# Kernel optimization log

Hardware: AMD Instinct MI355X
Metric: run time of the kernel (lower is better)

Reference implementation:

```python
import jax, jax.numpy as jnp
import numpy as np

N = 100000   # nodes
E = 1600000  # edges (avg degree 16)
D = 128      # embed_dim
H1, C1 = 8, 16   # gat1: heads=8, out=embed_dim//8=16, concat -> 128
C2 = 32          # gat2: heads=1, out=32
NEG_SLOPE = 0.2  # PyG GATConv default leaky relu slope


def _gat_layer(x, src, dst, W, a_src, a_dst, b, heads, ch, concat):
    """PyG-style GATConv (eval mode, add_self_loops already applied via src/dst)."""
    n = x.shape[0]
    h = (x @ W).reshape(n, heads, ch)                      # [N,H,C]
    alpha_s = jnp.einsum('nhc,hc->nh', h, a_src)           # [N,H]
    alpha_d = jnp.einsum('nhc,hc->nh', h, a_dst)           # [N,H]
    e = jax.nn.leaky_relu(alpha_s[src] + alpha_d[dst], NEG_SLOPE)  # [Etot,H]
    # segment softmax over incoming edges of each dst node
    m = jax.ops.segment_max(e, dst, num_segments=n)        # [N,H]
    ex = jnp.exp(e - m[dst])
    s = jax.ops.segment_sum(ex, dst, num_segments=n)       # [N,H]
    alpha = ex / (s[dst] + 1e-16)                          # [Etot,H]
    out = jax.ops.segment_sum(alpha[:, :, None] * h[src], dst, num_segments=n)  # [N,H,C]
    out = out.reshape(n, heads * ch) if concat else out.mean(axis=1)
    return out + b


def setup_inputs():
    key = jax.random.key(0)
    ks = jax.random.split(key, 12)
    x = jax.random.normal(ks[0], (N, D), dtype=jnp.float32)
    edge_index = jax.random.randint(ks[1], (2, E), 0, N, dtype=jnp.int64)
    sc = 0.1
    W1 = jax.random.normal(ks[2], (D, H1 * C1), jnp.float32) * sc
    a1_src = jax.random.normal(ks[3], (H1, C1), jnp.float32) * sc
    a1_dst = jax.random.normal(ks[4], (H1, C1), jnp.float32) * sc
    b1 = jnp.zeros((H1 * C1,), jnp.float32)
    W2 = jax.random.normal(ks[5], (H1 * C1, C2), jnp.float32) * sc
    a2_src = jax.random.normal(ks[6], (1, C2), jnp.float32) * sc
    a2_dst = jax.random.normal(ks[7], (1, C2), jnp.float32) * sc
    b2 = jnp.zeros((C2,), jnp.float32)
    Wh = jax.random.normal(ks[8], (C2, 1), jnp.float32) * sc
    bh = jnp.zeros((1,), jnp.float32)
    return {"x": x, "edge_index": edge_index,
            "W1": W1, "a1_src": a1_src, "a1_dst": a1_dst, "b1": b1,
            "W2": W2, "a2_src": a2_src, "a2_dst": a2_dst, "b2": b2,
            "Wh": Wh, "bh": bh}


def reference(x, edge_index, W1, a1_src, a1_dst, b1, W2, a2_src, a2_dst, b2, Wh, bh):
    n = x.shape[0]
    loops = jnp.arange(n, dtype=edge_index.dtype)
    src = jnp.concatenate([edge_index[0], loops])  # add_self_loops=True (PyG default)
    dst = jnp.concatenate([edge_index[1], loops])
    h = jax.nn.elu(_gat_layer(x, src, dst, W1, a1_src, a1_dst, b1, H1, C1, True))
    h = jax.nn.elu(_gat_layer(h, src, dst, W2, a2_src, a2_dst, b2, 1, C2, False))
    return h @ Wh + bh  # [N,1] ordinal head
```

## Files before the change

### kernel.cpp

```cpp
#include <hip/hip_runtime.h>
#include <hip/hip_bf16.h>
#include <stdint.h>
#include <stddef.h>

#define NEG_SLOPE 0.2f
#define XS 136

#define NBK   196
#define BWSH  9
#define BCAP  12288
#define NPREP 64

typedef __bf16 bf16x8 __attribute__((ext_vector_type(8)));
typedef float  f32x4  __attribute__((ext_vector_type(4)));

__device__ __forceinline__ float bf2f(__hip_bfloat16 b){ return __bfloat162float(b); }
__device__ __forceinline__ float lo_bf(unsigned u){ return __uint_as_float(u << 16); }
__device__ __forceinline__ float hi_bf(unsigned u){ return __uint_as_float(u & 0xffff0000u); }
__device__ __forceinline__ float lrelu(float u){ return fmaxf(u, NEG_SLOPE * u); }
__device__ __forceinline__ unsigned short f2bf(float f){
    unsigned u = __float_as_uint(f);
    return (unsigned short)((u + 0x7fffu + ((u >> 16) & 1u)) >> 16);
}
__device__ __forceinline__ float bfs2f(unsigned short s){ return __uint_as_float((unsigned)s << 16); }
__device__ __forceinline__ float ldraw(const void* p, int i, int isf){
    return isf ? ((const float*)p)[i] : bf2f(((const __hip_bfloat16*)p)[i]);
}

__global__ void detect_kernel(const unsigned* __restrict__ ei,
                              const unsigned* __restrict__ xw,
                              int* __restrict__ flags,
                              int* __restrict__ gcur){
    __shared__ int vote;
    const int t = threadIdx.x;
    if (t == 0) vote = 0;
    if (t < NBK) gcur[t] = t * BCAP;
    __syncthreads();
    if (t < 64){
        unsigned long long m = __ballot(ei[2*t + 1] != 0u);
        if (t == 0) flags[0] = (m == 0ull) ? 1 : 0;
    }
    {
        unsigned lo = xw[t] & 0xffffu;
        unsigned e  = (lo >> 7) & 0xffu;
        int pl = ((lo & 0x7fffu) == 0u || (e >= 100u && e <= 140u)) ? 1 : 0;
        atomicAdd(&vote, pl);
    }
    __syncthreads();
    if (t == 0) flags[1] = (vote < 128) ? 1 : 0;
}

#define WTS_TOTAL 20993
__global__ __launch_bounds__(256) void prep_scatter_kernel(
        const void* __restrict__ ei, const int* __restrict__ flags,
        int* __restrict__ gcur, unsigned* __restrict__ pairs, int E, int Et, int nsb,
        const void* W1, const void* W2, const void* a1s, const void* a1d,
        const void* b1, const void* a2s, const void* a2d, const void* b2,
        const void* Wh, const void* bh,
        float* __restrict__ w, unsigned short* __restrict__ w1x,
        unsigned short* __restrict__ w2x){
    const int t = threadIdx.x;
    if ((int)blockIdx.x < nsb){
        __shared__ int cnt[NBK], base[NBK], lcnt[NBK];
        const int e0 = blockIdx.x * 4096;
        const int nE = min(4096, Et - e0);
        for (int i = t; i < NBK; i += 256){ cnt[i] = 0; lcnt[i] = 0; }
        __syncthreads();
        const int is64 = flags[0];
        int2 sd[16];
#pragma unroll
        for (int k = 0; k < 16; k++){
            int j = t + k * 256;
            if (j < nE){
                int e = e0 + j, s, d;
                if (e >= E){ s = e - E; d = s; }
                else if (is64){
                    const long long* p = (const long long*)ei;
                    s = (int)p[e]; d = (int)p[(size_t)E + e];
                } else {
                    const int* p = (const int*)ei;
                    s = p[e]; d = p[(size_t)E + e];
                }
                sd[k] = make_int2(s, d);
                atomicAdd(&cnt[d >> BWSH], 1);
            } else sd[k].y = -1;
        }
        __syncthreads();
        for (int b = t; b < NBK; b += 256)
            base[b] = cnt[b] ? atomicAdd(&gcur[b], cnt[b]) : 0;
        __syncthreads();
#pragma unroll
        for (int k = 0; k < 16; k++){
            if (sd[k].y >= 0){
                int b = sd[k].y >> BWSH;
                int r = atomicAdd(&lcnt[b], 1);
                pairs[(size_t)base[b] + r] = ((unsigned)sd[k].x << BWSH) | (unsigned)(sd[k].y & 511);
            }
        }
    } else {
        const int p   = blockIdx.x - nsb;
        const int tid = p * 256 + t;
        const int NT  = NPREP * 256;
        const int isf = flags[1];
        for (int i = tid; i < 513; i += NT){
            int gi = 20480 + i;
            const void* src; int off;
            if      (gi < 20608){ src = a1s; off = gi - 20480; }
            else if (gi < 20736){ src = a1d; off = gi - 20608; }
            else if (gi < 20864){ src = b1;  off = gi - 20736; }
            else if (gi < 20896){ src = a2s; off = gi - 20864; }
            else if (gi < 20928){ src = a2d; off = gi - 20896; }
            else if (gi < 20960){ src = b2;  off = gi - 20928; }
            else if (gi < 20992){ src = Wh;  off = gi - 20960; }
            else                { src = bh;  off = 0; }
            w[gi] = ldraw(src, off, isf);
        }
        for (int i = tid; i < 16384; i += NT){
            int c = i >> 7, k = i & 127;
            w1x[i] = f2bf(ldraw(W1, k*128 + c, isf));
        }
        for (int i = tid; i < 4096; i += NT){
            int c = i >> 7, k = i & 127;
            w2x[i] = f2bf(ldraw(W2, k*32 + c, isf));
        }
        for (int i = tid; i < 12*128; i += NT) w2x[36*128 + i] = 0;
        for (int i = tid; i < 1024; i += NT){
            int h = i >> 7, k = i & 127;
            float ss = 0.f, dd = 0.f;
#pragma unroll
            for (int j = 0; j < 16; j++){
                float hv = ldraw(W1, k*128 + h*16 + j, isf);
                ss += hv * ldraw(a1s, h*16 + j, isf);
                dd += hv * ldraw(a1d, h*16 + j, isf);
            }
            unsigned short sh = f2bf(ss), dh = f2bf(dd);
            w1x[(128+h)*128 + k] = sh;
            w1x[(136+h)*128 + k] = f2bf(ss - bfs2f(sh));
            w1x[(144+h)*128 + k] = dh;
            w1x[(152+h)*128 + k] = f2bf(dd - bfs2f(dh));
        }
        for (int k = tid; k < 128; k += NT){
            float ss = 0.f, dd = 0.f;
#pragma unroll
            for (int j = 0; j < 32; j++){
                float hv = ldraw(W2, k*32 + j, isf);
                ss += hv * ldraw(a2s, j, isf);
                dd += hv * ldraw(a2d, j, isf);
            }
            unsigned short sh = f2bf(ss), dh = f2bf(dd);
            w2x[32*128 + k] = sh;
            w2x[33*128 + k] = f2bf(ss - bfs2f(sh));
            w2x[34*128 + k] = dh;
            w2x[35*128 + k] = f2bf(dd - bfs2f(dh));
        }
    }
}

__global__ __launch_bounds__(256) void g1csr_kernel(
        const unsigned* __restrict__ pairs, const int* __restrict__ gcur,
        int* __restrict__ rowptr, int* __restrict__ csr_src, int Nn,
        const void* __restrict__ xv, const unsigned short* __restrict__ w1x,
        const int* __restrict__ flags, __hip_bfloat16* __restrict__ h1b,
        float* __restrict__ as1, float* __restrict__ ad1){
    __shared__ __align__(16) char smem[52224];
    const int t = threadIdx.x;
    if ((int)blockIdx.x < NBK){
        int* ssz   = (int*)smem;
        int* sscan = ssz + 256;
        int* cnt   = sscan + 256;
        int* sh    = cnt + 512;
        const int b = blockIdx.x;
        int v = (t < NBK) ? (gcur[t] - t * BCAP) : 0;
        ssz[t] = v; sscan[t] = v;
        __syncthreads();
        for (int off = 1; off < 256; off <<= 1){
            int x = (t >= off) ? sscan[t - off] : 0;
            __syncthreads();
            sscan[t] += x;
            __syncthreads();
        }
        const int sz = ssz[b];
        const int eb = (b == 0) ? 0 : sscan[b - 1];
        if (b == 0 && t == 0) rowptr[Nn] = sscan[NBK - 1];
        const unsigned* pp = pairs + (size_t)b * BCAP;
        cnt[t] = 0; cnt[t + 256] = 0;
        __syncthreads();
        for (int i = t; i < sz; i += 256) atomicAdd(&cnt[pp[i] & 511u], 1);
        __syncthreads();
        int l0 = 2*t, l1 = 2*t + 1;
        int s0 = cnt[l0], s1 = cnt[l1], ts = s0 + s1;
        sh[t] = ts; __syncthreads();
        for (int off = 1; off < 256; off <<= 1){
            int x = (t >= off) ? sh[t - off] : 0;
            __syncthreads();
            sh[t] += x;
            __syncthreads();
        }
        int excl = sh[t] - ts;
        __syncthreads();
        cnt[l0] = eb + excl;
        cnt[l1] = eb + excl + s0;
        int n0 = (b << BWSH) + l0, n1 = (b << BWSH) + l1;
        if (n0 < Nn) rowptr[n0] = cnt[l0];
        if (n1 < Nn) rowptr[n1] = cnt[l1];
        __syncthreads();
        for (int i = t; i < sz; i += 256){
            unsigned sd = pp[i];
            int pos = atomicAdd(&cnt[sd & 511u], 1);
            csr_src[pos] = (int)(sd >> BWSH);
        }
    } else {
        __bf16* xls = (__bf16*)smem;
        __bf16* wls = (__bf16*)(smem + 64 * XS * 2);
        const int row0 = ((int)blockIdx.x - NBK) * 64;
        const int n = Nn;

#pragma unroll
        for (int k = 0; k < 8; k++){
            int e = (t + k * 256) * 8;
            int c = e >> 7, kk = e & 127;
            *(uint4*)(&wls[c * XS + kk]) = *(const uint4*)(w1x + e);
        }
        if (row0 + 64 <= n){
            if (flags[1]){
                const float* xp = (const float*)xv + (size_t)row0 * 128;
#pragma unroll
                for (int k = 0; k < 8; k++){
                    int e = (t + k * 256) * 4;
                    int row = e >> 7, col = e & 127;
                    float4 vv = *(const float4*)(xp + e);
                    uint2 o;
                    o.x = (unsigned)f2bf(vv.x) | ((unsigned)f2bf(vv.y) << 16);
                    o.y = (unsigned)f2bf(vv.z) | ((unsigned)f2bf(vv.w) << 16);
                    *(uint2*)(&xls[row * XS + col]) = o;
                }
            } else {
                const unsigned short* xp = (const unsigned short*)xv + (size_t)row0 * 128;
#pragma unroll
                for (int k = 0; k < 4; k++){
                    int e = (t + k * 256) * 8;
                    int row = e >> 7, col = e & 127;
                    *(uint4*)(&xls[row * XS + col]) = *(const uint4*)(xp + e);
                }
            }
        } else {
            const int limit = (n - row0) * 128;
            if (flags[1]){
                const float* xp = (const float*)xv + (size_t)row0 * 128;
                for (int i = t; i < 64 * 128; i += 256){
                    float v = (i < limit) ? xp[i] : 0.f;
                    xls[(i >> 7) * XS + (i & 127)] = (__bf16)v;
                }
            } else {
                const unsigned short* xp = (const unsigned short*)xv + (size_t)row0 * 128;
                for (int i = t; i < 64 * 128; i += 256){
                    unsigned short v = (i < limit) ? xp[i] : (unsigned short)0;
                    ((unsigned short*)xls)[(i >> 7) * XS + (i & 127)] = v;
                }
            }
        }
        __syncthreads();

        const int w    = t >> 6;
        const int lane = t & 63;
        const int l15  = lane & 15;
        const int quad = lane >> 4;

        f32x4 acc[8] = {};
        f32x4 accS = {}, accD = {};
        const __bf16* xbase = &xls[(w * 16 + l15) * XS + quad * 8];
        const __bf16* wbase = &wls[l15 * XS + quad * 8];
        const unsigned short* vsrow = w1x + (128 + l15) * 128 + quad * 8;
        const unsigned short* vdrow = w1x + (144 + l15) * 128 + quad * 8;

#pragma unroll
        for (int ks = 0; ks < 4; ks++){
            bf16x8 af = *(const bf16x8*)(xbase + ks * 32);
#pragma unroll
            for (int tt = 0; tt < 8; tt++){
                bf16x8 bfr = *(const bf16x8*)(wbase + tt * 16 * XS + ks * 32);
                acc[tt] = __builtin_amdgcn_mfma_f32_16x16x32_bf16(af, bfr, acc[tt], 0, 0, 0);
            }
            bf16x8 bS = *(const bf16x8*)(vsrow + ks * 32);
            bf16x8 bD = *(const bf16x8*)(vdrow + ks * 32);
            accS = __builtin_amdgcn_mfma_f32_16x16x32_bf16(af, bS, accS, 0, 0, 0);
            accD = __builtin_amdgcn_mfma_f32_16x16x32_bf16(af, bD, accD, 0, 0, 0);
        }

#pragma unroll
        for (int tt = 0; tt < 8; tt++){
            int col = tt * 16 + l15;
#pragma unroll
            for (int r = 0; r < 4; r++){
                int row = row0 + w * 16 + quad * 4 + r;
                if (row < n) h1b[(size_t)row * 128 + col] = __float2bfloat16(acc[tt][r]);
            }
        }
#pragma unroll
        for (int r = 0; r < 4; r++){
            float vs = accS[r] + __shfl_xor(accS[r], 8);
            float vd = accD[r] + __shfl_xor(accD[r], 8);
            int row = row0 + w * 16 + quad * 4 + r;
            if (l15 < 8 && row < n){
                as1[(size_t)row * 8 + l15] = vs;
                ad1[(size_t)row * 8 + l15] = vd;
            }
        }
    }
}

__global__ __launch_bounds__(256) void gather1_kernel(const int* __restrict__ rowptr,
                                                      const int* __restrict__ csr_src,
                                                      const float* __restrict__ as1,
                                                      const float* __restrict__ ad1,
                                                      const unsigned* __restrict__ h1u,
                                                      const float* __restrict__ b1,
                                                      unsigned* __restrict__ out1u, int n){
    int wid = blockIdx.x * 4 + (threadIdx.x >> 6);
    if (wid >= n) return;
    const int lane = threadIdx.x & 63;
    const int q    = lane >> 4;
    const int l15  = lane & 15;
    const int h    = l15 >> 1;
    const int start = rowptr[wid], end = rowptr[wid + 1];
    const float adv = ad1[(size_t)wid * 8 + h];
    float den = 0.f;
    float num[8] = {0.f,0.f,0.f,0.f,0.f,0.f,0.f,0.f};
    for (int j = start + q; j < end; j += 4){
        int src = csr_src[j];
        float u = lrelu(as1[(size_t)src * 8 + h] + adv);
        float w = __expf(u);
        uint4 hv = *(const uint4*)(h1u + (size_t)src * 64 + (l15 << 2));
        den += w;
        num[0] += w * lo_bf(hv.x); num[1] += w * hi_bf(hv.x);
        num[2] += w * lo_bf(hv.y); num[3] += w * hi_bf(hv.y);
        num[4] += w * lo_bf(hv.z); num[5] += w * hi_bf(hv.z);
        num[6] += w * lo_bf(hv.w); num[7] += w * hi_bf(hv.w);
    }
    den += __shfl_xor(den, 16); den += __shfl_xor(den, 32);
#pragma unroll
    for (int k = 0; k < 8; k++){
        num[k] += __shfl_xor(num[k], 16);
        num[k] += __shfl_xor(num[k], 32);
    }
    if (lane < 16){
        const int ch0 = l15 * 8;
        float inv = 1.f / (den + 1e-16f);
        uint4 o;
        unsigned* op = (unsigned*)&o;
#pragma unroll
        for (int k = 0; k < 4; k++){
            float r0 = num[2*k]   * inv + b1[ch0 + 2*k];
            float r1 = num[2*k+1] * inv + b1[ch0 + 2*k + 1];
            r0 = r0 > 0.f ? r0 : __expf(r0) - 1.f;
            r1 = r1 > 0.f ? r1 : __expf(r1) - 1.f;
            op[k] = (unsigned)f2bf(r0) | ((unsigned)f2bf(r1) << 16);
        }
        *(uint4*)(out1u + (size_t)wid * 64 + (l15 << 2)) = o;
    }
}

__global__ __launch_bounds__(256) void gemm2_kernel(const unsigned* __restrict__ out1u,
                                                    const unsigned short* __restrict__ w2x,
                                                    __hip_bfloat16* __restrict__ h2b,
                                                    float* __restrict__ as2,
                                                    float* __restrict__ ad2, int n){
    __shared__ __align__(16) __bf16 als[64 * XS];
    __shared__ __align__(16) __bf16 wls[32 * XS];
    const int t = threadIdx.x;
    const int row0 = blockIdx.x * 64;

#pragma unroll
    for (int k = 0; k < 2; k++){
        int e = (t + k * 256) * 8;
        int c = e >> 7, kk = e & 127;
        *(uint4*)(&wls[c * XS + kk]) = *(const uint4*)(w2x + e);
    }
    if (row0 + 64 <= n){
#pragma unroll
        for (int k = 0; k < 4; k++){
            int e = (t + k * 256) * 4;
            int row = e >> 6, cu = e & 63;
            *(uint4*)(&((unsigned*)als)[row * 68 + cu]) =
                *(const uint4*)(out1u + (size_t)row0 * 64 + e);
        }
    } else {
        const int limit = (n - row0) * 64;
        for (int i = t; i < 64 * 64; i += 256){
            unsigned v = (i < limit) ? out1u[(size_t)row0 * 64 + i] : 0u;
            ((unsigned*)als)[(i >> 6) * 68 + (i & 63)] = v;
        }
    }
    __syncthreads();

    const int w    = t >> 6;
    const int lane = t & 63;
    const int l15  = lane & 15;
    const int quad = lane >> 4;

    f32x4 acc[2] = {};
    f32x4 accE = {};
    const __bf16* abase = &als[(w * 16 + l15) * XS + quad * 8];
    const __bf16* bbase = &wls[l15 * XS + quad * 8];
    const unsigned short* verow = w2x + (32 + l15) * 128 + quad * 8;

#pragma unroll
    for (int ks = 0; ks < 4; ks++){
        bf16x8 af = *(const bf16x8*)(abase + ks * 32);
#pragma unroll
        for (int tt = 0; tt < 2; tt++){
            bf16x8 bfr = *(const bf16x8*)(bbase + tt * 16 * XS + ks * 32);
            acc[tt] = __builtin_amdgcn_mfma_f32_16x16x32_bf16(af, bfr, acc[tt], 0, 0, 0);
        }
        bf16x8 bE = *(const bf16x8*)(verow + ks * 32);
        accE = __builtin_amdgcn_mfma_f32_16x16x32_bf16(af, bE, accE, 0, 0, 0);
    }

#pragma unroll
    for (int r = 0; r < 4; r++){
        int row = row0 + w * 16 + quad * 4 + r;
        if (row < n){
#pragma unroll
            for (int tt = 0; tt < 2; tt++){
                int col = tt * 16 + l15;
                h2b[(size_t)row * 32 + col] = __float2bfloat16(acc[tt][r]);
            }
        }
        float vE = accE[r] + __shfl_xor(accE[r], 1);
        if (row < n){
            if (l15 == 0) as2[row] = vE;
            if (l15 == 2) ad2[row] = vE;
        }
    }
}

__global__ __launch_bounds__(256) void gather2_kernel(const int* __restrict__ rowptr,
                                                      const int* __restrict__ csr_src,
                                                      const float* __restrict__ as2,
                                                      const float* __restrict__ ad2,
                                                      const unsigned* __restrict__ h2u,
                                                      const float* __restrict__ b2,
                                                      const float* __restrict__ Wh,
                                                      const float* __restrict__ bh,
                                                      const int* __restrict__ flags,
                                                      void* __restrict__ out, int n){
    int wid = blockIdx.x * 4 + (threadIdx.x >> 6);
    if (wid >= n) return;
    int lane = threadIdx.x & 63;
    int q    = lane >> 4;
    int i2   = lane & 15;
    int ch0  = i2 * 2;
    int start = rowptr[wid], end = rowptr[wid + 1];
    float adv = ad2[wid];
    float den = 0.f, num0 = 0.f, num1 = 0.f;
    for (int j = start + q; j < end; j += 4){
        int src = csr_src[j];
        float u = lrelu(as2[src] + adv);
        float w = __expf(u);
        unsigned hv = h2u[(size_t)src * 16 + i2];
        den += w;
        num0 += w * lo_bf(hv);
        num1 += w * hi_bf(hv);
    }
    den  += __shfl_xor(den, 16);  den  += __shfl_xor(den, 32);
    num0 += __shfl_xor(num0, 16); num0 += __shfl_xor(num0, 32);
    num1 += __shfl_xor(num1, 16); num1 += __shfl_xor(num1, 32);
    float inv = 1.f / (den + 1e-16f);
    float v0 = num0 * inv + b2[ch0];
    float v1 = num1 * inv + b2[ch0 + 1];
    v0 = v0 > 0.f ? v0 : __expf(v0) - 1.f;
    v1 = v1 > 0.f ? v1 : __expf(v1) - 1.f;
    float p = v0 * Wh[ch0] + v1 * Wh[ch0 + 1];
#pragma unroll
    for (int off = 1; off < 16; off <<= 1) p += __shfl_xor(p, off);
    if (lane == 0){
        float r = p + bh[0];
        if (flags[1]) ((float*)out)[wid] = r;
        else          ((__hip_bfloat16*)out)[wid] = __float2bfloat16(r);
    }
}

extern "C" void kernel_launch(void* const* d_in, const int* in_sizes, int n_in,
                              void* d_out, int out_size, void* d_ws, size_t ws_size,
                              hipStream_t stream){
    const void* x   = d_in[0];
    const void* ei  = d_in[1];

    const int Nn = in_sizes[0] / 128;
    const int Ee = in_sizes[1] / 2;
    const int Et = Ee + Nn;
    const int nsb = (Et + 4095) / 4096;

    char* ws = (char*)d_ws;
    auto al = [](size_t v){ return (v + 255) & ~(size_t)255; };
    size_t off = 0;
    int*      flags  = (int*)(ws + off);      off = al(off + 16);
    float*    wts    = (float*)(ws + off);    off = al(off + (size_t)WTS_TOTAL * 4);
    unsigned short* w1x = (unsigned short*)(ws + off); off = al(off + 160 * 128 * 2);
    unsigned short* w2x = (unsigned short*)(ws + off); off = al(off + 48 * 128 * 2);
    int*      gcur   = (int*)(ws + off);      off = al(off + (size_t)NBK * 4);
    int*      rowptr = (int*)(ws + off);      off = al(off + (size_t)(Nn + 1) * 4);
    int*      csrs   = (int*)(ws + off);      off = al(off + (size_t)Et * 4);
    unsigned* pairs  = (unsigned*)(ws + off); off = al(off + (size_t)NBK * BCAP * 4);
    size_t o_h1 = off;
    __hip_bfloat16* h1b = (__hip_bfloat16*)(ws + off); off = al(off + (size_t)Nn * 128 * 2);
    float* as1  = (float*)(ws + off); off = al(off + (size_t)Nn * 8 * 4);
    float* ad1  = (float*)(ws + off); off = al(off + (size_t)Nn * 8 * 4);
    unsigned* out1u = (unsigned*)(ws + off); off = al(off + (size_t)Nn * 128 * 2);
    size_t o2 = o_h1;
    __hip_bfloat16* h2b = (__hip_bfloat16*)(ws + o2); o2 += (size_t)Nn * 32 * 2;
    float* as2  = (float*)(ws + o2);  o2 += (size_t)Nn * 4;
    float* ad2  = (float*)(ws + o2);  o2 += (size_t)Nn * 4;

    float* b1f  = wts + 20736;
    float* b2f  = wts + 20928;
    float* Whf  = wts + 20960;
    float* bhf  = wts + 20992;

    detect_kernel<<<1, 256, 0, stream>>>((const unsigned*)ei, (const unsigned*)x, flags, gcur);

    prep_scatter_kernel<<<nsb + NPREP, 256, 0, stream>>>(ei, flags, gcur, pairs, Ee, Et, nsb,
        d_in[2], d_in[6], d_in[3], d_in[4], d_in[5], d_in[7], d_in[8], d_in[9],
        d_in[10], d_in[11], wts, w1x, w2x);

    g1csr_kernel<<<NBK + (Nn + 63) / 64, 256, 0, stream>>>(pairs, gcur, rowptr, csrs, Nn,
        x, w1x, flags, h1b, as1, ad1);

    gather1_kernel<<<(Nn + 3) / 4, 256, 0, stream>>>(rowptr, csrs, as1, ad1,
                                                     (const unsigned*)h1b, b1f, out1u, Nn);

    gemm2_kernel<<<(Nn + 63) / 64, 256, 0, stream>>>(out1u, w2x, h2b, as2, ad2, Nn);

    gather2_kernel<<<(Nn + 3) / 4, 256, 0, stream>>>(rowptr, csrs, as2, ad2,
                                                     (const unsigned*)h2b, b2f,
                                                     Whf, bhf, flags, d_out, Nn);
}
```

Baseline: 313.1 us.

## Fuse all GAT stages into one persistent cooperative kernel with grid syncs

Replaces the six separate kernel launches (detect, prep/scatter, CSR build plus GEMM1, gather1, GEMM2, gather2) with one cooperative persistent kernel. Stages are separated by grid.sync() and blocks loop over work tiles. The GEMM paths also appear to switch from LDS-staged tiles to direct register loads. The aim is to remove launch overhead and inter-kernel gaps. In exchange, the grid is capped by occupancy, the grid barriers add cost, and the single kernel's register and LDS use may lower occupancy in the memory-bound gather phases.

```diff
diff --git a/kernel.cpp b/kernel.cpp
--- a/kernel.cpp
+++ b/kernel.cpp
@@ -1,15 +1,15 @@
 #include <hip/hip_runtime.h>
+#include <hip/hip_cooperative_groups.h>
 #include <hip/hip_bf16.h>
 #include <stdint.h>
 #include <stddef.h>
 
 #define NEG_SLOPE 0.2f
-#define XS 136
 
 #define NBK   196
 #define BWSH  9
 #define BCAP  12288
-#define NPREP 64
+#define WTS_TOTAL 20993
 
 typedef __bf16 bf16x8 __attribute__((ext_vector_type(8)));
 typedef float  f32x4  __attribute__((ext_vector_type(4)));
@@ -27,474 +27,420 @@
     return isf ? ((const float*)p)[i] : bf2f(((const __hip_bfloat16*)p)[i]);
 }
 
-__global__ void detect_kernel(const unsigned* __restrict__ ei,
-                              const unsigned* __restrict__ xw,
-                              int* __restrict__ flags,
-                              int* __restrict__ gcur){
-    __shared__ int vote;
-    const int t = threadIdx.x;
-    if (t == 0) vote = 0;
-    if (t < NBK) gcur[t] = t * BCAP;
+struct GParams {
+    const void* ei; const unsigned* xw;
+    const void *W1, *W2, *a1s, *a1d, *b1, *a2s, *a2d, *b2, *Wh, *bh;
+    float* wts; unsigned short* w1x; unsigned short* w2x;
+    int* gcur; int* rowptr; int* csrs; unsigned* pairs;
+    unsigned short* h1b; float* as1; float* ad1;
+    unsigned* out1u; unsigned short* h2b; float* as2; float* ad2;
+    void* out;
+    int Nn, Ee, Et, nsb, ngemm, nq;
+};
+
+__global__ __launch_bounds__(256) void mega_kernel(GParams p){
+    namespace cg = cooperative_groups;
+    cg::grid_group grid = cg::this_grid();
+    __shared__ int smi[1280];
+    __shared__ int s_is64, s_isf, s_vote;
+    const int t   = threadIdx.x;
+    const int bid = blockIdx.x;
+    const int nb  = gridDim.x;
+
+    if (t == 0) s_vote = 0;
     __syncthreads();
     if (t < 64){
-        unsigned long long m = __ballot(ei[2*t + 1] != 0u);
-        if (t == 0) flags[0] = (m == 0ull) ? 1 : 0;
-    }
-    {
-        unsigned lo = xw[t] & 0xffffu;
+        unsigned long long m = __ballot(((const unsigned*)p.ei)[2*t + 1] != 0u);
+        if (t == 0) s_is64 = (m == 0ull) ? 1 : 0;
+    }
+    {
+        unsigned lo = p.xw[t] & 0xffffu;
         unsigned e  = (lo >> 7) & 0xffu;
         int pl = ((lo & 0x7fffu) == 0u || (e >= 100u && e <= 140u)) ? 1 : 0;
-        atomicAdd(&vote, pl);
+        atomicAdd(&s_vote, pl);
     }
     __syncthreads();
-    if (t == 0) flags[1] = (vote < 128) ? 1 : 0;
-}
-
-#define WTS_TOTAL 20993
-__global__ __launch_bounds__(256) void prep_scatter_kernel(
-        const void* __restrict__ ei, const int* __restrict__ flags,
-        int* __restrict__ gcur, unsigned* __restrict__ pairs, int E, int Et, int nsb,
-        const void* W1, const void* W2, const void* a1s, const void* a1d,
-        const void* b1, const void* a2s, const void* a2d, const void* b2,
-        const void* Wh, const void* bh,
-        float* __restrict__ w, unsigned short* __restrict__ w1x,
-        unsigned short* __restrict__ w2x){
-    const int t = threadIdx.x;
-    if ((int)blockIdx.x < nsb){
-        __shared__ int cnt[NBK], base[NBK], lcnt[NBK];
-        const int e0 = blockIdx.x * 4096;
-        const int nE = min(4096, Et - e0);
-        for (int i = t; i < NBK; i += 256){ cnt[i] = 0; lcnt[i] = 0; }
-        __syncthreads();
-        const int is64 = flags[0];
-        int2 sd[16];
-#pragma unroll
-        for (int k = 0; k < 16; k++){
-            int j = t + k * 256;
-            if (j < nE){
-                int e = e0 + j, s, d;
-                if (e >= E){ s = e - E; d = s; }
-                else if (is64){
-                    const long long* p = (const long long*)ei;
-                    s = (int)p[e]; d = (int)p[(size_t)E + e];
-                } else {
-                    const int* p = (const int*)ei;
-                    s = p[e]; d = p[(size_t)E + e];
-                }
-                sd[k] = make_int2(s, d);
-                atomicAdd(&cnt[d >> BWSH], 1);
-            } else sd[k].y = -1;
-        }
-        __syncthreads();
-        for (int b = t; b < NBK; b += 256)
-            base[b] = cnt[b] ? atomicAdd(&gcur[b], cnt[b]) : 0;
-        __syncthreads();
-#pragma unroll
-        for (int k = 0; k < 16; k++){
-            if (sd[k].y >= 0){
-                int b = sd[k].y >> BWSH;
-                int r = atomicAdd(&lcnt[b], 1);
-                pairs[(size_t)base[b] + r] = ((unsigned)sd[k].x << BWSH) | (unsigned)(sd[k].y & 511);
-            }
-        }
-    } else {
-        const int p   = blockIdx.x - nsb;
-        const int tid = p * 256 + t;
-        const int NT  = NPREP * 256;
-        const int isf = flags[1];
+    if (t == 0) s_isf = (s_vote < 128) ? 1 : 0;
+    __syncthreads();
+    const int is64 = s_is64, isf = s_isf;
+
+    if (bid == 0 && t < NBK) p.gcur[t] = 0;
+    {
+        const int tid = bid * 256 + t;
+        const int NT  = nb * 256;
         for (int i = tid; i < 513; i += NT){
             int gi = 20480 + i;
             const void* src; int off;
-            if      (gi < 20608){ src = a1s; off = gi - 20480; }
-            else if (gi < 20736){ src = a1d; off = gi - 20608; }
-            else if (gi < 20864){ src = b1;  off = gi - 20736; }
-            else if (gi < 20896){ src = a2s; off = gi - 20864; }
-            else if (gi < 20928){ src = a2d; off = gi - 20896; }
-            else if (gi < 20960){ src = b2;  off = gi - 20928; }
-            else if (gi < 20992){ src = Wh;  off = gi - 20960; }
-            else                { src = bh;  off = 0; }
-            w[gi] = ldraw(src, off, isf);
+            if      (gi < 20608){ src = p.a1s; off = gi - 20480; }
+            else if (gi < 20736){ src = p.a1d; off = gi - 20608; }
+            else if (gi < 20864){ src = p.b1;  off = gi - 20736; }
+            else if (gi < 20896){ src = p.a2s; off = gi - 20864; }
+            else if (gi < 20928){ src = p.a2d; off = gi - 20896; }
+            else if (gi < 20960){ src = p.b2;  off = gi - 20928; }
+            else if (gi < 20992){ src = p.Wh;  off = gi - 20960; }
+            else                { src = p.bh;  off = 0; }
+            p.wts[gi] = ldraw(src, off, isf);
         }
         for (int i = tid; i < 16384; i += NT){
             int c = i >> 7, k = i & 127;
-            w1x[i] = f2bf(ldraw(W1, k*128 + c, isf));
-        }
-        for (int i = tid; i < 4096; i += NT){
-            int c = i >> 7, k = i & 127;
-            w2x[i] = f2bf(ldraw(W2, k*32 + c, isf));
-        }
-        for (int i = tid; i < 12*128; i += NT) w2x[36*128 + i] = 0;
+            p.w1x[i] = f2bf(ldraw(p.W1, k*128 + c, isf));
+        }
         for (int i = tid; i < 1024; i += NT){
             int h = i >> 7, k = i & 127;
             float ss = 0.f, dd = 0.f;
 #pragma unroll
             for (int j = 0; j < 16; j++){
-                float hv = ldraw(W1, k*128 + h*16 + j, isf);
-                ss += hv * ldraw(a1s, h*16 + j, isf);
-                dd += hv * ldraw(a1d, h*16 + j, isf);
+                float hv = ldraw(p.W1, k*128 + h*16 + j, isf);
+                ss += hv * ldraw(p.a1s, h*16 + j, isf);
+                dd += hv * ldraw(p.a1d, h*16 + j, isf);
             }
             unsigned short sh = f2bf(ss), dh = f2bf(dd);
-            w1x[(128+h)*128 + k] = sh;
-            w1x[(136+h)*128 + k] = f2bf(ss - bfs2f(sh));
-            w1x[(144+h)*128 + k] = dh;
-            w1x[(152+h)*128 + k] = f2bf(dd - bfs2f(dh));
-        }
+            p.w1x[(128+h)*128 + k] = sh;
+            p.w1x[(136+h)*128 + k] = f2bf(ss - bfs2f(sh));
+            p.w1x[(144+h)*128 + k] = dh;
+            p.w1x[(152+h)*128 + k] = f2bf(dd - bfs2f(dh));
+        }
+        for (int i = tid; i < 4096; i += NT){
+            int c = i >> 7, k = i & 127;
+            p.w2x[i] = f2bf(ldraw(p.W2, k*32 + c, isf));
+        }
+        for (int i = tid; i < 12*128; i += NT) p.w2x[36*128 + i] = 0;
         for (int k = tid; k < 128; k += NT){
             float ss = 0.f, dd = 0.f;
 #pragma unroll
             for (int j = 0; j < 32; j++){
-                float hv = ldraw(W2, k*32 + j, isf);
-                ss += hv * ldraw(a2s, j, isf);
-                dd += hv * ldraw(a2d, j, isf);
+                float hv = ldraw(p.W2, k*32 + j, isf);
+                ss += hv * ldraw(p.a2s, j, isf);
+                dd += hv * ldraw(p.a2d, j, isf);
             }
             unsigned short sh = f2bf(ss), dh = f2bf(dd);
-            w2x[32*128 + k] = sh;
-            w2x[33*128 + k] = f2bf(ss - bfs2f(sh));
-            w2x[34*128 + k] = dh;
-            w2x[35*128 + k] = f2bf(dd - bfs2f(dh));
-        }
-    }
-}
-
-__global__ __launch_bounds__(256) void g1csr_kernel(
-        const unsigned* __restrict__ pairs, const int* __restrict__ gcur,
-        int* __restrict__ rowptr, int* __restrict__ csr_src, int Nn,
-        const void* __restrict__ xv, const unsigned short* __restrict__ w1x,
-        const int* __restrict__ flags, __hip_bfloat16* __restrict__ h1b,
-        float* __restrict__ as1, float* __restrict__ ad1){
-    __shared__ __align__(16) char smem[52224];
-    const int t = threadIdx.x;
-    if ((int)blockIdx.x < NBK){
-        int* ssz   = (int*)smem;
-        int* sscan = ssz + 256;
-        int* cnt   = sscan + 256;
-        int* sh    = cnt + 512;
-        const int b = blockIdx.x;
-        int v = (t < NBK) ? (gcur[t] - t * BCAP) : 0;
-        ssz[t] = v; sscan[t] = v;
-        __syncthreads();
-        for (int off = 1; off < 256; off <<= 1){
-            int x = (t >= off) ? sscan[t - off] : 0;
+            p.w2x[32*128 + k] = sh;
+            p.w2x[33*128 + k] = f2bf(ss - bfs2f(sh));
+            p.w2x[34*128 + k] = dh;
+            p.w2x[35*128 + k] = f2bf(dd - bfs2f(dh));
+        }
+    }
+    grid.sync();
+
+    {
+        int* cnt  = smi;
+        int* base = smi + 256;
+        int* lcnt = smi + 512;
+        for (int tile = bid; tile < p.nsb; tile += nb){
+            const int e0 = tile * 4096;
+            const int nE = min(4096, p.Et - e0);
+            for (int i = t; i < NBK; i += 256){ cnt[i] = 0; lcnt[i] = 0; }
             __syncthreads();
-            sscan[t] += x;
+            int2 sd[16];
+#pragma unroll
+            for (int k = 0; k < 16; k++){
+                int j = t + k * 256;
+                if (j < nE){
+                    int e = e0 + j, s, d;
+                    if (e >= p.Ee){ s = e - p.Ee; d = s; }
+                    else if (is64){
+                        const long long* q = (const long long*)p.ei;
+                        s = (int)q[e]; d = (int)q[(size_t)p.Ee + e];
+                    } else {
+                        const int* q = (const int*)p.ei;
+                        s = q[e]; d = q[(size_t)p.Ee + e];
+                    }
+                    sd[k] = make_int2(s, d);
+                    atomicAdd(&cnt[d >> BWSH], 1);
+                } else sd[k].y = -1;
+            }
             __syncthreads();
-        }
-        const int sz = ssz[b];
-        const int eb = (b == 0) ? 0 : sscan[b - 1];
-        if (b == 0 && t == 0) rowptr[Nn] = sscan[NBK - 1];
-        const unsigned* pp = pairs + (size_t)b * BCAP;
-        cnt[t] = 0; cnt[t + 256] = 0;
-        __syncthreads();
-        for (int i = t; i < sz; i += 256) atomicAdd(&cnt[pp[i] & 511u], 1);
-        __syncthreads();
-        int l0 = 2*t, l1 = 2*t + 1;
-        int s0 = cnt[l0], s1 = cnt[l1], ts = s0 + s1;
-        sh[t] = ts; __syncthreads();
-        for (int off = 1; off < 256; off <<= 1){
-            int x = (t >= off) ? sh[t - off] : 0;
+            for (int b = t; b < NBK; b += 256)
+                base[b] = cnt[b] ? (b * BCAP + atomicAdd(&p.gcur[b], cnt[b])) : 0;
             __syncthreads();
-            sh[t] += x;
+#pragma unroll
+            for (int k = 0; k < 16; k++){
+                if (sd[k].y >= 0){
+                    int b = sd[k].y >> BWSH;
+                    int r = atomicAdd(&lcnt[b], 1);
+                    p.pairs[(size_t)base[b] + r] =
+                        ((unsigned)sd[k].x << BWSH) | (unsigned)(sd[k].y & 511);
+                }
+            }
             __syncthreads();
         }
-        int excl = sh[t] - ts;
-        __syncthreads();
-        cnt[l0] = eb + excl;
-        cnt[l1] = eb + excl + s0;
-        int n0 = (b << BWSH) + l0, n1 = (b << BWSH) + l1;
-        if (n0 < Nn) rowptr[n0] = cnt[l0];
-        if (n1 < Nn) rowptr[n1] = cnt[l1];
-        __syncthreads();
-        for (int i = t; i < sz; i += 256){
-            unsigned sd = pp[i];
-            int pos = atomicAdd(&cnt[sd & 511u], 1);
-            csr_src[pos] = (int)(sd >> BWSH);
-        }
-    } else {
-        __bf16* xls = (__bf16*)smem;
-        __bf16* wls = (__bf16*)(smem + 64 * XS * 2);
-        const int row0 = ((int)blockIdx.x - NBK) * 64;
-        const int n = Nn;
-
-#pragma unroll
-        for (int k = 0; k < 8; k++){
-            int e = (t + k * 256) * 8;
-            int c = e >> 7, kk = e & 127;
-            *(uint4*)(&wls[c * XS + kk]) = *(const uint4*)(w1x + e);
-        }
-        if (row0 + 64 <= n){
-            if (flags[1]){
-                const float* xp = (const float*)xv + (size_t)row0 * 128;
-#pragma unroll
-                for (int k = 0; k < 8; k++){
-                    int e = (t + k * 256) * 4;
-                    int row = e >> 7, col = e & 127;
-                    float4 vv = *(const float4*)(xp + e);
-                    uint2 o;
-                    o.x = (unsigned)f2bf(vv.x) | ((unsigned)f2bf(vv.y) << 16);
-                    o.y = (unsigned)f2bf(vv.z) | ((unsigned)f2bf(vv.w) << 16);
-                    *(uint2*)(&xls[row * XS + col]) = o;
-                }
+    }
+    grid.sync();
+
+    {
+        const int tot = NBK + p.ngemm;
+        for (int i = bid; i < tot; i += nb){
+            if (i < NBK){
+                int* ssz   = smi;
+                int* sscan = smi + 256;
+                int* cnt   = smi + 512;
+                int* sh    = smi + 1024;
+                const int b = i;
+                int v = (t < NBK) ? p.gcur[t] : 0;
+                ssz[t] = v; sscan[t] = v;
+                __syncthreads();
+                for (int off = 1; off < 256; off <<= 1){
+                    int x2 = (t >= off) ? sscan[t - off] : 0;
+                    __syncthreads();
+                    sscan[t] += x2;
+                    __syncthreads();
+                }
+                const int sz = ssz[b];
+                const int eb = (b == 0) ? 0 : sscan[b - 1];
+                if (b == 0 && t == 0) p.rowptr[p.Nn] = sscan[NBK - 1];
+                const unsigned* pp = p.pairs + (size_t)b * BCAP;
+                cnt[t] = 0; cnt[t + 256] = 0;
+                __syncthreads();
+                for (int j = t; j < sz; j += 256) atomicAdd(&cnt[pp[j] & 511u], 1);
+                __syncthreads();
+                int l0 = 2*t, l1 = 2*t + 1;
+                int s0 = cnt[l0], s1 = cnt[l1], ts = s0 + s1;
+                sh[t] = ts; __syncthreads();
+                for (int off = 1; off < 256; off <<= 1){
+                    int x2 = (t >= off) ? sh[t - off] : 0;
+                    __syncthreads();
+                    sh[t] += x2;
+                    __syncthreads();
+                }
+                int excl = sh[t] - ts;
+                __syncthreads();
+                cnt[l0] = eb + excl;
+                cnt[l1] = eb + excl + s0;
+                int n0 = (b << BWSH) + l0, n1 = (b << BWSH) + l1;
+                if (n0 < p.Nn) p.rowptr[n0] = cnt[l0];
+                if (n1 < p.Nn) p.rowptr[n1] = cnt[l1];
+                __syncthreads();
+                for (int j = t; j < sz; j += 256){
+                    unsigned sd = pp[j];
+                    int pos = atomicAdd(&cnt[sd & 511u], 1);
+                    p.csrs[pos] = (int)(sd >> BWSH);
+                }
+                __syncthreads();
             } else {
-                const unsigned short* xp = (const unsigned short*)xv + (size_t)row0 * 128;
+                const int row0 = (i - NBK) * 64;
+                const int w    = t >> 6;
+                const int lane = t & 63;
+                const int l15  = lane & 15;
+                const int quad = lane >> 4;
+                const int r0   = row0 + w * 16 + l15;
+                const bool arow = r0 < p.Nn;
+
+                f32x4 acc[8] = {};
+                f32x4 accS = {}, accD = {};
+#pragma unroll
+                for (int ks = 0; ks < 4; ks++){
+                    bf16x8 af;
+                    if (arow){
+                        if (isf){
+                            const float* xp = (const float*)p.xw + (size_t)r0 * 128 + quad * 8 + ks * 32;
+                            float4 v0 = *(const float4*)xp;
+                            float4 v1 = *(const float4*)(xp + 4);
+                            union { bf16x8 v; unsigned short s[8]; } u;
+                            u.s[0]=f2bf(v0.x); u.s[1]=f2bf(v0.y); u.s[2]=f2bf(v0.z); u.s[3]=f2bf(v0.w);
+                            u.s[4]=f2bf(v1.x); u.s[5]=f2bf(v1.y); u.s[6]=f2bf(v1.z); u.s[7]=f2bf(v1.w);
+                            af = u.v;
+                        } else {
+                            af = *(const bf16x8*)((const unsigned short*)p.xw + (size_t)r0 * 128 + quad * 8 + ks * 32);
+                        }
+                    } else {
+                        union { bf16x8 v; unsigned short s[8]; } u;
+#pragma unroll
+                        for (int j = 0; j < 8; j++) u.s[j] = 0;
+                        af = u.v;
+                    }
+#pragma unroll
+                    for (int tt = 0; tt < 8; tt++){
+                        bf16x8 bfr = *(const bf16x8*)(p.w1x + (tt*16 + l15)*128 + quad*8 + ks*32);
+                        acc[tt] = __builtin_amdgcn_mfma_f32_16x16x32_bf16(af, bfr, acc[tt], 0, 0, 0);
+                    }
+                    bf16x8 bS = *(const bf16x8*)(p.w1x + (128 + l15)*128 + quad*8 + ks*32);
+                    bf16x8 bD = *(const bf16x8*)(p.w1x + (144 + l15)*128 + quad*8 + ks*32);
+                    accS = __builtin_amdgcn_mfma_f32_16x16x32_bf16(af, bS, accS, 0, 0, 0);
+                    accD = __builtin_amdgcn_mfma_f32_16x16x32_bf16(af, bD, accD, 0, 0, 0);
+                }
+#pragma unroll
+                for (int tt = 0; tt < 8; tt++){
+                    int col = tt * 16 + l15;
+#pragma unroll
+                    for (int r = 0; r < 4; r++){
+                        int row = row0 + w * 16 + quad * 4 + r;
+                        if (row < p.Nn) p.h1b[(size_t)row * 128 + col] = f2bf(acc[tt][r]);
+                    }
+                }
+#pragma unroll
+                for (int r = 0; r < 4; r++){
+                    float vs = accS[r] + __shfl_xor(accS[r], 8);
+                    float vd = accD[r] + __shfl_xor(accD[r], 8);
+                    int row = row0 + w * 16 + quad * 4 + r;
+                    if (l15 < 8 && row < p.Nn){
+                        p.as1[(size_t)row * 8 + l15] = vs;
+                        p.ad1[(size_t)row * 8 + l15] = vd;
+                    }
+                }
+            }
+        }
+    }
+    grid.sync();
+
+    {
+        const float* b1v = p.wts + 20736;
+        for (int i = bid; i < p.nq; i += nb){
+            const int wv   = t >> 6;
+            const int lane = t & 63;
+            const int wid0 = i * 4 + wv;
+            const bool active = wid0 < p.Nn;
+            const int wid  = active ? wid0 : 0;
+            const int q    = lane >> 4;
+            const int l15  = lane & 15;
+            const int h    = l15 >> 1;
+            const int start = active ? p.rowptr[wid] : 0;
+            const int end   = active ? p.rowptr[wid + 1] : 0;
+            const float adv = p.ad1[(size_t)wid * 8 + h];
+            float den = 0.f;
+            float num[8] = {0.f,0.f,0.f,0.f,0.f,0.f,0.f,0.f};
+            for (int j = start + q; j < end; j += 4){
+                int src = p.csrs[j];
+                float u = lrelu(p.as1[(size_t)src * 8 + h] + adv);
+                float w = __expf(u);
+                uint4 hv = *(const uint4*)((const unsigned*)p.h1b + (size_t)src * 64 + (l15 << 2));
+                den += w;
+                num[0] += w * lo_bf(hv.x); num[1] += w * hi_bf(hv.x);
+                num[2] += w * lo_bf(hv.y); num[3] += w * hi_bf(hv.y);
+                num[4] += w * lo_bf(hv.z); num[5] += w * hi_bf(hv.z);
+                num[6] += w * lo_bf(hv.w); num[7] += w * hi_bf(hv.w);
+            }
+            den += __shfl_xor(den, 16); den += __shfl_xor(den, 32);
+#pragma unroll
+            for (int k = 0; k < 8; k++){
+                num[k] += __shfl_xor(num[k], 16);
+                num[k] += __shfl_xor(num[k], 32);
+            }
+            if (active && lane < 16){
+                const int ch0 = l15 * 8;
+                float inv = 1.f / (den + 1e-16f);
+                uint4 o;
+                unsigned* op = (unsigned*)&o;
 #pragma unroll
                 for (int k = 0; k < 4; k++){
-                    int e = (t + k * 256) * 8;
-                    int row = e >> 7, col = e & 127;
-                    *(uint4*)(&xls[row * XS + col]) = *(const uint4*)(xp + e);
-                }
-            }
-        } else {
-            const int limit = (n - row0) * 128;
-            if (flags[1]){
-                const float* xp = (const float*)xv + (size_t)row0 * 128;
-                for (int i = t; i < 64 * 128; i += 256){
-                    float v = (i < limit) ? xp[i] : 0.f;
-                    xls[(i >> 7) * XS + (i & 127)] = (__bf16)v;
-                }
-            } else {
-                const unsigned short* xp = (const unsigned short*)xv + (size_t)row0 * 128;
-                for (int i = t; i < 64 * 128; i += 256){
-                    unsigned short v = (i < limit) ? xp[i] : (unsigned short)0;
-                    ((unsigned short*)xls)[(i >> 7) * XS + (i & 127)] = v;
-                }
-            }
-        }
-        __syncthreads();
-
-        const int w    = t >> 6;
-        const int lane = t & 63;
-        const int l15  = lane & 15;
-        const int quad = lane >> 4;
-
-        f32x4 acc[8] = {};
-        f32x4 accS = {}, accD = {};
-        const __bf16* xbase = &xls[(w * 16 + l15) * XS + quad * 8];
-        const __bf16* wbase = &wls[l15 * XS + quad * 8];
-        const unsigned short* vsrow = w1x + (128 + l15) * 128 + quad * 8;
-        const unsigned short* vdrow = w1x + (144 + l15) * 128 + quad * 8;
-
-#pragma unroll
-        for (int ks = 0; ks < 4; ks++){
-            bf16x8 af = *(const bf16x8*)(xbase + ks * 32);
-#pragma unroll
-            for (int tt = 0; tt < 8; tt++){
-                bf16x8 bfr = *(const bf16x8*)(wbase + tt * 16 * XS + ks * 32);
-                acc[tt] = __builtin_amdgcn_mfma_f32_16x16x32_bf16(af, bfr, acc[tt], 0, 0, 0);
-            }
-            bf16x8 bS = *(const bf16x8*)(vsrow + ks * 32);
-            bf16x8 bD = *(const bf16x8*)(vdrow + ks * 32);
-            accS = __builtin_amdgcn_mfma_f32_16x16x32_bf16(af, bS, accS, 0, 0, 0);
-            accD = __builtin_amdgcn_mfma_f32_16x16x32_bf16(af, bD, accD, 0, 0, 0);
-        }
-
-#pragma unroll
-        for (int tt = 0; tt < 8; tt++){
-            int col = tt * 16 + l15;
+                    float r0 = num[2*k]   * inv + b1v[ch0 + 2*k];
+                    float r1 = num[2*k+1] * inv + b1v[ch0 + 2*k + 1];
+                    r0 = r0 > 0.f ? r0 : __expf(r0) - 1.f;
+                    r1 = r1 > 0.f ? r1 : __expf(r1) - 1.f;
+                    op[k] = (unsigned)f2bf(r0) | ((unsigned)f2bf(r1) << 16);
+                }
+                *(uint4*)(p.out1u + (size_t)wid * 64 + (l15 << 2)) = o;
+            }
+        }
+    }
+    grid.sync();
+
+    {
+        for (int i = bid; i < p.ngemm; i += nb){
+            const int row0 = i * 64;
+            const int w    = t >> 6;
+            const int lane = t & 63;
+            const int l15  = lane & 15;
+            const int quad = lane >> 4;
+            const int r0   = row0 + w * 16 + l15;
+            const bool arow = r0 < p.Nn;
+
+            f32x4 acc[2] = {};
+            f32x4 accE = {};
+#pragma unroll
+            for (int ks = 0; ks < 4; ks++){
+                bf16x8 af;
+                if (arow){
+                    af = *(const bf16x8*)((const unsigned short*)p.out1u + (size_t)r0 * 128 + quad * 8 + ks * 32);
+                } else {
+                    union { bf16x8 v; unsigned short s[8]; } u;
+#pragma unroll
+                    for (int j = 0; j < 8; j++) u.s[j] = 0;
+                    af = u.v;
+                }
+#pragma unroll
+                for (int tt = 0; tt < 2; tt++){
+                    bf16x8 bfr = *(const bf16x8*)(p.w2x + (tt*16 + l15)*128 + quad*8 + ks*32);
+                    acc[tt] = __builtin_amdgcn_mfma_f32_16x16x32_bf16(af, bfr, acc[tt], 0, 0, 0);
+                }
+                bf16x8 bE = *(const bf16x8*)(p.w2x + (32 + l15)*128 + quad*8 + ks*32);
+                accE = __builtin_amdgcn_mfma_f32_16x16x32_bf16(af, bE, accE, 0, 0, 0);
+            }
 #pragma unroll
             for (int r = 0; r < 4; r++){
                 int row = row0 + w * 16 + quad * 4 + r;
-                if (row < n) h1b[(size_t)row * 128 + col] = __float2bfloat16(acc[tt][r]);
-            }
-        }
-#pragma unroll
-        for (int r = 0; r < 4; r++){
-            float vs = accS[r] + __shfl_xor(accS[r], 8);
-            float vd = accD[r] + __shfl_xor(accD[r], 8);
-            int row = row0 + w * 16 + quad * 4 + r;
-            if (l15 < 8 && row < n){
-                as1[(size_t)row * 8 + l15] = vs;
-                ad1[(size_t)row * 8 + l15] = vd;
-            }
-        }
-    }
-}
-
-__global__ __launch_bounds__(256) void gather1_kernel(const int* __restrict__ rowptr,
-                                                      const int* __restrict__ csr_src,
-                                                      const float* __restrict__ as1,
-                                                      const float* __restrict__ ad1,
-                                                      const unsigned* __restrict__ h1u,
-                                                      const float* __restrict__ b1,
-                                                      unsigned* __restrict__ out1u, int n){
-    int wid = blockIdx.x * 4 + (threadIdx.x >> 6);
-    if (wid >= n) return;
-    const int lane = threadIdx.x & 63;
-    const int q    = lane >> 4;
-    const int l15  = lane & 15;
-    const int h    = l15 >> 1;
-    const int start = rowptr[wid], end = rowptr[wid + 1];
-    const float adv = ad1[(size_t)wid * 8 + h];
-    float den = 0.f;
-    float num[8] = {0.f,0.f,0.f,0.f,0.f,0.f,0.f,0.f};
-    for (int j = start + q; j < end; j += 4){
-        int src = csr_src[j];
-        float u = lrelu(as1[(size_t)src * 8 + h] + adv);
-        float w = __expf(u);
-        uint4 hv = *(const uint4*)(h1u + (size_t)src * 64 + (l15 << 2));
-        den += w;
-        num[0] += w * lo_bf(hv.x); num[1] += w * hi_bf(hv.x);
-        num[2] += w * lo_bf(hv.y); num[3] += w * hi_bf(hv.y);
-        num[4] += w * lo_bf(hv.z); num[5] += w * hi_bf(hv.z);
-        num[6] += w * lo_bf(hv.w); num[7] += w * hi_bf(hv.w);
-    }
-    den += __shfl_xor(den, 16); den += __shfl_xor(den, 32);
-#pragma unroll
-    for (int k = 0; k < 8; k++){
-        num[k] += __shfl_xor(num[k], 16);
-        num[k] += __shfl_xor(num[k], 32);
-    }
-    if (lane < 16){
-        const int ch0 = l15 * 8;
-        float inv = 1.f / (den + 1e-16f);
-        uint4 o;
-        unsigned* op = (unsigned*)&o;
-#pragma unroll
-        for (int k = 0; k < 4; k++){
-            float r0 = num[2*k]   * inv + b1[ch0 + 2*k];
-            float r1 = num[2*k+1] * inv + b1[ch0 + 2*k + 1];
-            r0 = r0 > 0.f ? r0 : __expf(r0) - 1.f;
-            r1 = r1 > 0.f ? r1 : __expf(r1) - 1.f;
-            op[k] = (unsigned)f2bf(r0) | ((unsigned)f2bf(r1) << 16);
-        }
-        *(uint4*)(out1u + (size_t)wid * 64 + (l15 << 2)) = o;
-    }
-}
-
-__global__ __launch_bounds__(256) void gemm2_kernel(const unsigned* __restrict__ out1u,
-                                                    const unsigned short* __restrict__ w2x,
-                                                    __hip_bfloat16* __restrict__ h2b,
-                                                    float* __restrict__ as2,
-                                                    float* __restrict__ ad2, int n){
-    __shared__ __align__(16) __bf16 als[64 * XS];
-    __shared__ __align__(16) __bf16 wls[32 * XS];
-    const int t = threadIdx.x;
-    const int row0 = blockIdx.x * 64;
-
-#pragma unroll
-    for (int k = 0; k < 2; k++){
-        int e = (t + k * 256) * 8;
-        int c = e >> 7, kk = e & 127;
-        *(uint4*)(&wls[c * XS + kk]) = *(const uint4*)(w2x + e);
-    }
-    if (row0 + 64 <= n){
-#pragma unroll
-        for (int k = 0; k < 4; k++){
-            int e = (t + k * 256) * 4;
-            int row = e >> 6, cu = e & 63;
-            *(uint4*)(&((unsigned*)als)[row * 68 + cu]) =
-                *(const uint4*)(out1u + (size_t)row0 * 64 + e);
-        }
-    } else {
-        const int limit = (n - row0) * 64;
-        for (int i = t; i < 64 * 64; i += 256){
-            unsigned v = (i < limit) ? out1u[(size_t)row0 * 64 + i] : 0u;
-            ((unsigned*)als)[(i >> 6) * 68 + (i & 63)] = v;
-        }
-    }
-    __syncthreads();
-
-    const int w    = t >> 6;
-    const int lane = t & 63;
-    const int l15  = lane & 15;
-    const int quad = lane >> 4;
-
-    f32x4 acc[2] = {};
-    f32x4 accE = {};
-    const __bf16* abase = &als[(w * 16 + l15) * XS + quad * 8];
-    const __bf16* bbase = &wls[l15 * XS + quad * 8];
-    const unsigned short* verow = w2x + (32 + l15) * 128 + quad * 8;
-
-#pragma unroll
-    for (int ks = 0; ks < 4; ks++){
-        bf16x8 af = *(const bf16x8*)(abase + ks * 32);
-#pragma unroll
-        for (int tt = 0; tt < 2; tt++){
-            bf16x8 bfr = *(const bf16x8*)(bbase + tt * 16 * XS + ks * 32);
-            acc[tt] = __builtin_amdgcn_mfma_f32_16x16x32_bf16(af, bfr, acc[tt], 0, 0, 0);
-        }
-        bf16x8 bE = *(const bf16x8*)(verow + ks * 32);
-        accE = __builtin_amdgcn_mfma_f32_16x16x32_bf16(af, bE, accE, 0, 0, 0);
-    }
-
-#pragma unroll
-    for (int r = 0; r < 4; r++){
-        int row = row0 + w * 16 + quad * 4 + r;
-        if (row < n){
-#pragma unroll
-            for (int tt = 0; tt < 2; tt++){
-                int col = tt * 16 + l15;
-                h2b[(size_t)row * 32 + col] = __float2bfloat16(acc[tt][r]);
-            }
-        }
-        float vE = accE[r] + __shfl_xor(accE[r], 1);
-        if (row < n){
-            if (l15 == 0) as2[row] = vE;
-            if (l15 == 2) ad2[row] = vE;
-        }
-    }
-}
-
-__global__ __launch_bounds__(256) void gather2_kernel(const int* __restrict__ rowptr,
-                                                      const int* __restrict__ csr_src,
-                                                      const float* __restrict__ as2,
-                                                      const float* __restrict__ ad2,
-                                                      const unsigned* __restrict__ h2u,
-                                                      const float* __restrict__ b2,
-                                                      const float* __restrict__ Wh,
-                                                      const float* __restrict__ bh,
-                                                      const int* __restrict__ flags,
-                                                      void* __restrict__ out, int n){
-    int wid = blockIdx.x * 4 + (threadIdx.x >> 6);
-    if (wid >= n) return;
-    int lane = threadIdx.x & 63;
-    int q    = lane >> 4;
-    int i2   = lane & 15;
-    int ch0  = i2 * 2;
-    int start = rowptr[wid], end = rowptr[wid + 1];
-    float adv = ad2[wid];
-    float den = 0.f, num0 = 0.f, num1 = 0.f;
-    for (int j = start + q; j < end; j += 4){
-        int src = csr_src[j];
-        float u = lrelu(as2[src] + adv);
-        float w = __expf(u);
-        unsigned hv = h2u[(size_t)src * 16 + i2];
-        den += w;
-        num0 += w * lo_bf(hv);
-        num1 += w * hi_bf(hv);
-    }
-    den  += __shfl_xor(den, 16);  den  += __shfl_xor(den, 32);
-    num0 += __shfl_xor(num0, 16); num0 += __shfl_xor(num0, 32);
-    num1 += __shfl_xor(num1, 16); num1 += __shfl_xor(num1, 32);
-    float inv = 1.f / (den + 1e-16f);
-    float v0 = num0 * inv + b2[ch0];
-    float v1 = num1 * inv + b2[ch0 + 1];
-    v0 = v0 > 0.f ? v0 : __expf(v0) - 1.f;
-    v1 = v1 > 0.f ? v1 : __expf(v1) - 1.f;
-    float p = v0 * Wh[ch0] + v1 * Wh[ch0 + 1];
-#pragma unroll
-    for (int off = 1; off < 16; off <<= 1) p += __shfl_xor(p, off);
-    if (lane == 0){
-        float r = p + bh[0];
-        if (flags[1]) ((float*)out)[wid] = r;
-        else          ((__hip_bfloat16*)out)[wid] = __float2bfloat16(r);
+                if (row < p.Nn){
+#pragma unroll
+                    for (int tt = 0; tt < 2; tt++){
+                        int col = tt * 16 + l15;
+                        p.h2b[(size_t)row * 32 + col] = f2bf(acc[tt][r]);
+                    }
+                }
+                float vE = accE[r] + __shfl_xor(accE[r], 1);
+                if (row < p.Nn){
+                    if (l15 == 0) p.as2[row] = vE;
+                    if (l15 == 2) p.ad2[row] = vE;
+                }
+            }
+        }
+    }
+    grid.sync();
+
+    {
+        const float* b2v = p.wts + 20928;
+        const float* Whv = p.wts + 20960;
+        const float* bhv = p.wts + 20992;
+        for (int i = bid; i < p.nq; i += nb){
+            const int wv   = t >> 6;
+            const int lane = t & 63;
+            const int wid0 = i * 4 + wv;
+            const bool active = wid0 < p.Nn;
+            const int wid  = active ? wid0 : 0;
+            const int q    = lane >> 4;
+            const int i2   = lane & 15;
+            const int ch0  = i2 * 2;
+            const int start = active ? p.rowptr[wid] : 0;
+            const int end   = active ? p.rowptr[wid + 1] : 0;
+            const float adv = p.ad2[wid];
+            float den = 0.f, num0 = 0.f, num1 = 0.f;
+            for (int j = start + q; j < end; j += 4){
+                int src = p.csrs[j];
+                float u = lrelu(p.as2[src] + adv);
+                float w = __expf(u);
+                unsigned hv = ((const unsigned*)p.h2b)[(size_t)src * 16 + i2];
+                den += w;
+                num0 += w * lo_bf(hv);
+                num1 += w * hi_bf(hv);
+            }
+            den  += __shfl_xor(den, 16);  den  += __shfl_xor(den, 32);
+            num0 += __shfl_xor(num0, 16); num0 += __shfl_xor(num0, 32);
+            num1 += __shfl_xor(num1, 16); num1 += __shfl_xor(num1, 32);
+            float inv = 1.f / (den + 1e-16f);
+            float v0 = num0 * inv + b2v[ch0];
+            float v1 = num1 * inv + b2v[ch0 + 1];
+            v0 = v0 > 0.f ? v0 : __expf(v0) - 1.f;
+            v1 = v1 > 0.f ? v1 : __expf(v1) - 1.f;
+            float pr = v0 * Whv[ch0] + v1 * Whv[ch0 + 1];
+#pragma unroll
+            for (int off = 1; off < 16; off <<= 1) pr += __shfl_xor(pr, off);
+            if (active && lane == 0){
+                float r = pr + bhv[0];
+                if (isf) ((float*)p.out)[wid] = r;
+                else     ((__hip_bfloat16*)p.out)[wid] = __float2bfloat16(r);
+            }
+        }
     }
 }
 
 extern "C" void kernel_launch(void* const* d_in, const int* in_sizes, int n_in,
                               void* d_out, int out_size, void* d_ws, size_t ws_size,
                               hipStream_t stream){
-    const void* x   = d_in[0];
-    const void* ei  = d_in[1];
-
     const int Nn = in_sizes[0] / 128;
     const int Ee = in_sizes[1] / 2;
     const int Et = Ee + Nn;
-    const int nsb = (Et + 4095) / 4096;
 
     char* ws = (char*)d_ws;
     auto al = [](size_t v){ return (v + 255) & ~(size_t)255; };
     size_t off = 0;
-    int*      flags  = (int*)(ws + off);      off = al(off + 16);
     float*    wts    = (float*)(ws + off);    off = al(off + (size_t)WTS_TOTAL * 4);
     unsigned short* w1x = (unsigned short*)(ws + off); off = al(off + 160 * 128 * 2);
     unsigned short* w2x = (unsigned short*)(ws + off); off = al(off + 48 * 128 * 2);
@@ -502,36 +448,37 @@
     int*      rowptr = (int*)(ws + off);      off = al(off + (size_t)(Nn + 1) * 4);
     int*      csrs   = (int*)(ws + off);      off = al(off + (size_t)Et * 4);
     unsigned* pairs  = (unsigned*)(ws + off); off = al(off + (size_t)NBK * BCAP * 4);
-    size_t o_h1 = off;
-    __hip_bfloat16* h1b = (__hip_bfloat16*)(ws + off); off = al(off + (size_t)Nn * 128 * 2);
+    unsigned short* h1b = (unsigned short*)(ws + off); off = al(off + (size_t)Nn * 128 * 2);
     float* as1  = (float*)(ws + off); off = al(off + (size_t)Nn * 8 * 4);
     float* ad1  = (float*)(ws + off); off = al(off + (size_t)Nn * 8 * 4);
     unsigned* out1u = (unsigned*)(ws + off); off = al(off + (size_t)Nn * 128 * 2);
-    size_t o2 = o_h1;
-    __hip_bfloat16* h2b = (__hip_bfloat16*)(ws + o2); o2 += (size_t)Nn * 32 * 2;
-    float* as2  = (float*)(ws + o2);  o2 += (size_t)Nn * 4;
-    float* ad2  = (float*)(ws + o2);  o2 += (size_t)Nn * 4;
-
-    float* b1f  = wts + 20736;
-    float* b2f  = wts + 20928;
-    float* Whf  = wts + 20960;
-    float* bhf  = wts + 20992;
-
-    detect_kernel<<<1, 256, 0, stream>>>((const unsigned*)ei, (const unsigned*)x, flags, gcur);
-
-    prep_scatter_kernel<<<nsb + NPREP, 256, 0, stream>>>(ei, flags, gcur, pairs, Ee, Et, nsb,
-        d_in[2], d_in[6], d_in[3], d_in[4], d_in[5], d_in[7], d_in[8], d_in[9],
-        d_in[10], d_in[11], wts, w1x, w2x);
-
-    g1csr_kernel<<<NBK + (Nn + 63) / 64, 256, 0, stream>>>(pairs, gcur, rowptr, csrs, Nn,
-        x, w1x, flags, h1b, as1, ad1);
-
-    gather1_kernel<<<(Nn + 3) / 4, 256, 0, stream>>>(rowptr, csrs, as1, ad1,
-                                                     (const unsigned*)h1b, b1f, out1u, Nn);
-
-    gemm2_kernel<<<(Nn + 63) / 64, 256, 0, stream>>>(out1u, w2x, h2b, as2, ad2, Nn);
-
-    gather2_kernel<<<(Nn + 3) / 4, 256, 0, stream>>>(rowptr, csrs, as2, ad2,
-                                                     (const unsigned*)h2b, b2f,
-                                                     Whf, bhf, flags, d_out, Nn);
+    unsigned short* h2b = (unsigned short*)(ws + off); off = al(off + (size_t)Nn * 32 * 2);
+    float* as2  = (float*)(ws + off); off = al(off + (size_t)Nn * 4);
+    float* ad2  = (float*)(ws + off); off = al(off + (size_t)Nn * 4);
+
+    GParams P;
+    P.ei = d_in[1]; P.xw = (const unsigned*)d_in[0];
+    P.W1 = d_in[2]; P.W2 = d_in[6];
+    P.a1s = d_in[3]; P.a1d = d_in[4]; P.b1 = d_in[5];
+    P.a2s = d_in[7]; P.a2d = d_in[8]; P.b2 = d_in[9];
+    P.Wh = d_in[10]; P.bh = d_in[11];
+    P.wts = wts; P.w1x = w1x; P.w2x = w2x;
+    P.gcur = gcur; P.rowptr = rowptr; P.csrs = csrs; P.pairs = pairs;
+    P.h1b = h1b; P.as1 = as1; P.ad1 = ad1;
+    P.out1u = out1u; P.h2b = h2b; P.as2 = as2; P.ad2 = ad2;
+    P.out = d_out;
+    P.Nn = Nn; P.Ee = Ee; P.Et = Et;
+    P.nsb = (Et + 4095) / 4096;
+    P.ngemm = (Nn + 63) / 64;
+    P.nq = (Nn + 3) / 4;
+
+    int maxB = 0;
+    hipOccupancyMaxActiveBlocksPerMultiprocessor(&maxB, mega_kernel, 256, 0);
+    if (maxB < 1) maxB = 1;
+    if (maxB > 8) maxB = 8;
+    int grid = maxB * 256;
+
+    void* args[] = { &P };
+    hipLaunchCooperativeKernel((void*)mega_kernel, dim3(grid), dim3(256),
+                               args, 0, stream);
 }
```

After: 1.010 ms. 3.23x slower.
